# Kernel optimization log

Measured on AMD Instinct MI355X. Metric: run time of the kernel, lower is better.

The kernel has to match this reference:

```python
import jax, jax.numpy as jnp
import numpy as np

AUX_LOSS_WEIGHT = 0.01
TOP_K = 2


def setup_inputs() -> dict:
    key = jax.random.key(0)
    k0, k1, k2, k3, k4 = jax.random.split(key, 5)
    B, S, H, I, E = 4, 2048, 1024, 2816, 8
    scale = 0.02
    x = jax.random.normal(k0, (B, S, H), dtype=jnp.float32)
    Wr = jax.random.normal(k1, (H, E), dtype=jnp.float32) * scale   # router
    Wg = jax.random.normal(k2, (E, H, I), dtype=jnp.float32) * scale  # gate proj per expert
    Wu = jax.random.normal(k3, (E, H, I), dtype=jnp.float32) * scale  # up proj per expert
    Wd = jax.random.normal(k4, (E, I, H), dtype=jnp.float32) * scale  # down proj per expert
    return {"x": x, "Wr": Wr, "Wg": Wg, "Wu": Wu, "Wd": Wd}


def reference(x, Wr, Wg, Wu, Wd):
    B, S, H = x.shape
    E = Wr.shape[1]
    xf = x.reshape(-1, H)                      # [T, H]

    # Router: softmax -> top-k -> renormalize top-k weights
    logits = xf @ Wr                           # [T, E]
    probs = jax.nn.softmax(logits, axis=-1)
    vals, idx = jax.lax.top_k(probs, TOP_K)    # [T, K]
    vals = vals / (vals.sum(axis=-1, keepdims=True) + 1e-9)

    # Aux load-balancing loss (matches torch: mean prob * mean one-hot load)
    oh = jax.nn.one_hot(idx, E, dtype=xf.dtype)        # [T, K, E]
    expert_load = oh.sum(axis=1).mean(axis=0)          # [E]
    expert_prob = probs.mean(axis=0)                   # [E]
    router_loss = E * jnp.sum(expert_prob * expert_load) * AUX_LOSS_WEIGHT

    # Per-token combine weight for each expert: c[t,e] = sum_k vals[t,k] * (idx[t,k]==e)
    comb = jnp.einsum('tk,tke->te', vals, oh)          # [T, E]

    # Loop over the small fixed set of experts (dense SwiGLU, masked-weighted combine;
    # identical math to gather -> expert -> weighted index_add scatter)
    def expert_step(acc, ew):
        wg, wu, wd, ce = ew                            # [H,I], [H,I], [I,H], [T]
        h = jax.nn.silu(xf @ wg) * (xf @ wu)           # [T, I]
        return acc + (h @ wd) * ce[:, None], None

    out, _ = jax.lax.scan(expert_step, jnp.zeros_like(xf), (Wg, Wu, Wd, comb.T))
    return out.reshape(B, S, H), router_loss
```

## Files before the change

kernel.cpp:

```cpp
#include <hip/hip_runtime.h>
#include <stdint.h>

#define T_TOK 8192
#define HD    1024
#define ID    2816
#define NE    8
#define RCAP  17408
#define NYT   (RCAP / 128)

typedef __bf16 bf16x8 __attribute__((ext_vector_type(8)));
typedef float  f32x4  __attribute__((ext_vector_type(4)));

__device__ __forceinline__ unsigned short f2bf(float f) {
  union { float f; unsigned u; } v; v.f = f;
  unsigned r = v.u + 0x7FFFu + ((v.u >> 16) & 1u);
  return (unsigned short)(r >> 16);
}

__device__ __forceinline__ void gl16(const void* g, void* l) {
  __builtin_amdgcn_global_load_lds((__attribute__((address_space(1))) void*)g,
                                   (__attribute__((address_space(3))) void*)l,
                                   16, 0, 0);
}

__global__ void k_prep(const float* __restrict__ x, const float* __restrict__ Wr,
                       const float* __restrict__ Wg, const float* __restrict__ Wu,
                       const float* __restrict__ Wd,
                       unsigned short* __restrict__ Wgt, unsigned short* __restrict__ Wut,
                       unsigned short* __restrict__ Wdt, unsigned short* __restrict__ xb,
                       int* __restrict__ cnt, float* __restrict__ psum,
                       int* __restrict__ tok_e, float* __restrict__ tok_w) {
  __shared__ __align__(16) unsigned short tl[64 * 64];
  __shared__ float bp[NE];
  __shared__ int bc[NE];
  const int bid = blockIdx.x;
  const int t = threadIdx.x;

  if (bid < 16896) {
    const int m = bid / 704, bx = bid - m * 704;
    const float* src; unsigned short* dst; int R, C;
    if (m < 8)       { src = Wg + (size_t)m * HD * ID;        dst = Wgt + (size_t)m * HD * ID;        R = HD; C = ID; }
    else if (m < 16) { src = Wu + (size_t)(m - 8) * HD * ID;  dst = Wut + (size_t)(m - 8) * HD * ID;  R = HD; C = ID; }
    else             { src = Wd + (size_t)(m - 16) * HD * ID; dst = Wdt + (size_t)(m - 16) * HD * ID; R = ID; C = HD; }
    const int tc = C / 64;
    const int tr = bx / tc, tcc = bx % tc;
    const int r0 = tr * 64, c0 = tcc * 64;
    const int rb = t >> 4;
    const int c4 = t & 15;
    const float* sp = src + (size_t)(r0 + rb * 4) * C + c0 + c4 * 4;
    float4 v[4];
#pragma unroll
    for (int i = 0; i < 4; ++i) v[i] = *(const float4*)(sp + (size_t)i * C);
    const float* vf = (const float*)v;
#pragma unroll
    for (int q = 0; q < 4; ++q) {
      const int c = c4 * 4 + q;
      ushort4 o;
      o.x = f2bf(vf[0 * 4 + q]); o.y = f2bf(vf[1 * 4 + q]);
      o.z = f2bf(vf[2 * 4 + q]); o.w = f2bf(vf[3 * 4 + q]);
      *(ushort4*)&tl[c * 64 + ((rb ^ (c & 15)) * 4)] = o;
    }
    __syncthreads();
    const int orow = t >> 2, seg = t & 3;
    __align__(16) unsigned short tmp[16];
#pragma unroll
    for (int mI = 0; mI < 4; ++mI) {
      const int s = seg * 4 + mI;
      *(ushort4*)&tmp[mI * 4] = *(const ushort4*)&tl[orow * 64 + ((s ^ (orow & 15)) * 4)];
    }
    unsigned short* dp = dst + (size_t)(c0 + orow) * R + r0 + seg * 16;
    ((uint4*)dp)[0] = ((const uint4*)tmp)[0];
    ((uint4*)dp)[1] = ((const uint4*)tmp)[1];
  } else {
    const int b = bid - 16896;
    if (t < NE) { bp[t] = 0.f; bc[t] = 0; }
    __syncthreads();
    const int lane = t & 63, w = t >> 6;
    const int tok = b * 4 + w;
    float acc[NE] = {0.f, 0.f, 0.f, 0.f, 0.f, 0.f, 0.f, 0.f};
    for (int h = lane; h < HD; h += 64) {
      const float xv = x[(size_t)tok * HD + h];
      xb[(size_t)tok * HD + h] = f2bf(xv);
      const float4 w0 = *(const float4*)(Wr + h * 8);
      const float4 w1 = *(const float4*)(Wr + h * 8 + 4);
      acc[0] += xv * w0.x; acc[1] += xv * w0.y; acc[2] += xv * w0.z; acc[3] += xv * w0.w;
      acc[4] += xv * w1.x; acc[5] += xv * w1.y; acc[6] += xv * w1.z; acc[7] += xv * w1.w;
    }
#pragma unroll
    for (int e = 0; e < NE; ++e)
      for (int off = 32; off > 0; off >>= 1)
        acc[e] += __shfl_xor(acc[e], off, 64);
    if (lane == 0) {
      float mx = acc[0];
      for (int e = 1; e < NE; ++e) mx = fmaxf(mx, acc[e]);
      float p[NE], s = 0.f;
      for (int e = 0; e < NE; ++e) { p[e] = __expf(acc[e] - mx); s += p[e]; }
      const float inv = 1.f / s;
      for (int e = 0; e < NE; ++e) p[e] *= inv;
      int e0 = 0;
      for (int e = 1; e < NE; ++e) if (p[e] > p[e0]) e0 = e;
      int e1 = (e0 == 0) ? 1 : 0;
      for (int e = 0; e < NE; ++e) if (e != e0 && p[e] > p[e1]) e1 = e;
      const float v0 = p[e0], v1 = p[e1];
      const float invs = 1.f / (v0 + v1 + 1e-9f);
      tok_e[2 * tok] = e0;          tok_e[2 * tok + 1] = e1;
      tok_w[2 * tok] = v0 * invs;   tok_w[2 * tok + 1] = v1 * invs;
      atomicAdd(&bc[e0], 1); atomicAdd(&bc[e1], 1);
      for (int e = 0; e < NE; ++e) atomicAdd(&bp[e], p[e]);
    }
    __syncthreads();
    if (t < NE) { atomicAdd(&cnt[t], bc[t]); atomicAdd(&psum[t], bp[t]); }
  }
}

__global__ void k_offsets(const int* __restrict__ cnt, const float* __restrict__ psum,
                          int* __restrict__ offp, int* __restrict__ pair_tok,
                          float* __restrict__ pair_w, float* __restrict__ loss_out) {
  __shared__ int soff[NE + 1], scnt[NE];
  if (threadIdx.x == 0) {
    int o = 0;
    for (int e = 0; e < NE; ++e) {
      soff[e] = o; scnt[e] = cnt[e];
      o += (scnt[e] + 127) & ~127;
    }
    soff[NE] = o;
    for (int e = 0; e <= NE; ++e) offp[e] = soff[e];
    float loss = 0.f;
    for (int e = 0; e < NE; ++e) loss += psum[e] * (float)scnt[e];
    loss *= (float)NE * 0.01f / ((float)T_TOK * (float)T_TOK);
    *loss_out = loss;
  }
  __syncthreads();
  for (int e = 0; e < NE; ++e) {
    const int base = soff[e] + scnt[e];
    const int n = soff[e + 1] - base;
    for (int j = threadIdx.x; j < n; j += blockDim.x) {
      pair_tok[base + j] = -1;
      pair_w[base + j] = 0.f;
    }
  }
}

__global__ void k_scatter(const int* __restrict__ tok_e, const float* __restrict__ tok_w,
                          const int* __restrict__ offp, int* __restrict__ cursor,
                          int* __restrict__ pair_tok, float* __restrict__ pair_w,
                          int* __restrict__ inv_p) {
  const int t = blockIdx.x * 256 + threadIdx.x;
#pragma unroll
  for (int k = 0; k < 2; ++k) {
    const int e = tok_e[2 * t + k];
    const int pos = atomicAdd(&cursor[e], 1);
    const int idx = offp[e] + pos;
    pair_tok[idx] = t;
    pair_w[idx] = tok_w[2 * t + k];
    inv_p[2 * t + k] = idx;
  }
}

__launch_bounds__(256, 2)
__global__ void k_stage1(const unsigned short* __restrict__ xb,
                         const unsigned short* __restrict__ Wgt,
                         const unsigned short* __restrict__ Wut,
                         const int* __restrict__ offp,
                         const int* __restrict__ pair_tok,
                         unsigned short* __restrict__ act) {
  __shared__ __align__(16) unsigned short lA[8192];
  __shared__ __align__(16) unsigned short lBg[8192];
  __shared__ __align__(16) unsigned short lBu[8192];
  __shared__ int toks[128];

  const int wg = blockIdx.x;
  const int ytile = wg % NYT;
  const int i0 = (wg / NYT) * 128;
  const int row0 = ytile * 128;
  if (row0 >= offp[8]) return;
  int e = 0;
  while (offp[e + 1] <= row0) ++e;
  const int tid = threadIdx.x;
  if (tid < 128) {
    const int tk = pair_tok[row0 + tid];
    toks[tid] = tk < 0 ? 0 : tk;
  }
  __syncthreads();

  const int lane = tid & 63, w = tid >> 6;
  const unsigned short* gA[4];
  const unsigned short* gBg[4];
  const unsigned short* gBu[4];
  unsigned ldso[4];
  const unsigned short* wgtE = Wgt + (size_t)e * ID * HD;
  const unsigned short* wutE = Wut + (size_t)e * ID * HD;
#pragma unroll
  for (int j = 0; j < 4; ++j) {
    const int row = (w * 4 + j) * 8 + (lane >> 3);
    const int kb = (lane & 7) ^ (row & 7);
    gA[j]  = xb + (size_t)toks[row] * HD + kb * 8;
    gBg[j] = wgtE + (size_t)(i0 + row) * HD + kb * 8;
    gBu[j] = wutE + (size_t)(i0 + row) * HD + kb * 8;
    ldso[j] = (unsigned)(w * 4 + j) * 512u;
  }

  const f32x4 zero = {0.f, 0.f, 0.f, 0.f};
  f32x4 accg[4][4], accu[4][4];
#pragma unroll
  for (int a = 0; a < 4; ++a)
#pragma unroll
    for (int b = 0; b < 4; ++b) { accg[a][b] = zero; accu[a][b] = zero; }

  const int wm = (w & 1) * 64, wn = (w >> 1) * 64;
  const int colm = lane & 15, quad = lane >> 4;

  for (int kt = 0; kt < HD / 64; ++kt) {
    __syncthreads();
    const int ko = kt * 64;
#pragma unroll
    for (int j = 0; j < 4; ++j) {
      gl16(gA[j] + ko,  &lA[ldso[j]]);
      gl16(gBg[j] + ko, &lBg[ldso[j]]);
      gl16(gBu[j] + ko, &lBu[ldso[j]]);
    }
    __syncthreads();
#pragma unroll
    for (int kk = 0; kk < 2; ++kk) {
      const int kbl = kk * 4 + quad;
      bf16x8 af[4], bg[4], bu[4];
#pragma unroll
      for (int mf = 0; mf < 4; ++mf) {
        const int r = wm + mf * 16 + colm;
        af[mf] = *(const bf16x8*)&lA[r * 64 + ((kbl ^ (r & 7)) * 8)];
      }
#pragma unroll
      for (int nf = 0; nf < 4; ++nf) {
        const int r = wn + nf * 16 + colm;
        const int o = r * 64 + ((kbl ^ (r & 7)) * 8);
        bg[nf] = *(const bf16x8*)&lBg[o];
        bu[nf] = *(const bf16x8*)&lBu[o];
      }
#pragma unroll
      for (int mf = 0; mf < 4; ++mf)
#pragma unroll
        for (int nf = 0; nf < 4; ++nf) {
          accg[mf][nf] = __builtin_amdgcn_mfma_f32_16x16x32_bf16(af[mf], bg[nf], accg[mf][nf], 0, 0, 0);
          accu[mf][nf] = __builtin_amdgcn_mfma_f32_16x16x32_bf16(af[mf], bu[nf], accu[mf][nf], 0, 0, 0);
        }
    }
  }

#pragma unroll
  for (int mf = 0; mf < 4; ++mf) {
#pragma unroll
    for (int r = 0; r < 4; ++r) {
      const int orow = row0 + wm + mf * 16 + quad * 4 + r;
      unsigned short* arow = act + (size_t)orow * ID + i0 + wn + colm;
#pragma unroll
      for (int nf = 0; nf < 4; ++nf) {
        const float g = accg[mf][nf][r];
        const float u = accu[mf][nf][r];
        const float h = (g / (1.f + __expf(-g))) * u;
        arow[nf * 16] = f2bf(h);
      }
    }
  }
}

__launch_bounds__(256, 2)
__global__ void k_stage2(const unsigned short* __restrict__ act,
                         const unsigned short* __restrict__ Wdt,
                         const int* __restrict__ offp,
                         float* __restrict__ contrib) {
  __shared__ __align__(16) unsigned short lA[8192];
  __shared__ __align__(16) unsigned short lB[8192];

  const int wg = blockIdx.x;
  const int ytile = wg % NYT;
  const int h0 = (wg / NYT) * 128;
  const int row0 = ytile * 128;
  if (row0 >= offp[8]) return;
  int e = 0;
  while (offp[e + 1] <= row0) ++e;
  const int tid = threadIdx.x;
  const int lane = tid & 63, w = tid >> 6;
  const unsigned short* gA[4];
  const unsigned short* gB[4];
  unsigned ldso[4];
  const unsigned short* wdE = Wdt + (size_t)e * HD * ID;
#pragma unroll
  for (int j = 0; j < 4; ++j) {
    const int row = (w * 4 + j) * 8 + (lane >> 3);
    const int kb = (lane & 7) ^ (row & 7);
    gA[j] = act + (size_t)(row0 + row) * ID + kb * 8;
    gB[j] = wdE + (size_t)(h0 + row) * ID + kb * 8;
    ldso[j] = (unsigned)(w * 4 + j) * 512u;
  }

  const f32x4 zero = {0.f, 0.f, 0.f, 0.f};
  f32x4 acc[4][4];
#pragma unroll
  for (int a = 0; a < 4; ++a)
#pragma unroll
    for (int b = 0; b < 4; ++b) acc[a][b] = zero;

  const int wm = (w & 1) * 64, wn = (w >> 1) * 64;
  const int colm = lane & 15, quad = lane >> 4;

  for (int kt = 0; kt < ID / 64; ++kt) {
    __syncthreads();
    const int ko = kt * 64;
#pragma unroll
    for (int j = 0; j < 4; ++j) {
      gl16(gA[j] + ko, &lA[ldso[j]]);
      gl16(gB[j] + ko, &lB[ldso[j]]);
    }
    __syncthreads();
#pragma unroll
    for (int kk = 0; kk < 2; ++kk) {
      const int kbl = kk * 4 + quad;
      bf16x8 af[4], bf_[4];
#pragma unroll
      for (int mf = 0; mf < 4; ++mf) {
        const int r = wm + mf * 16 + colm;
        af[mf] = *(const bf16x8*)&lA[r * 64 + ((kbl ^ (r & 7)) * 8)];
      }
#pragma unroll
      for (int nf = 0; nf < 4; ++nf) {
        const int r = wn + nf * 16 + colm;
        bf_[nf] = *(const bf16x8*)&lB[r * 64 + ((kbl ^ (r & 7)) * 8)];
      }
#pragma unroll
      for (int mf = 0; mf < 4; ++mf)
#pragma unroll
        for (int nf = 0; nf < 4; ++nf)
          acc[mf][nf] = __builtin_amdgcn_mfma_f32_16x16x32_bf16(af[mf], bf_[nf], acc[mf][nf], 0, 0, 0);
    }
  }

#pragma unroll
  for (int mf = 0; mf < 4; ++mf) {
#pragma unroll
    for (int r = 0; r < 4; ++r) {
      const int lrow = wm + mf * 16 + quad * 4 + r;
      float* crow = contrib + (size_t)(row0 + lrow) * HD + h0 + wn + colm;
#pragma unroll
      for (int nf = 0; nf < 4; ++nf)
        crow[nf * 16] = acc[mf][nf][r];
    }
  }
}

__global__ void k_combine(const float* __restrict__ contrib, const int* __restrict__ inv_p,
                          const float* __restrict__ tok_w, float* __restrict__ out) {
  const int t = blockIdx.x;
  const int h4 = threadIdx.x;
  const int p0 = inv_p[2 * t], p1 = inv_p[2 * t + 1];
  const float w0 = tok_w[2 * t], w1 = tok_w[2 * t + 1];
  const float4 a = ((const float4*)(contrib + (size_t)p0 * HD))[h4];
  const float4 b = ((const float4*)(contrib + (size_t)p1 * HD))[h4];
  float4 o;
  o.x = w0 * a.x + w1 * b.x;
  o.y = w0 * a.y + w1 * b.y;
  o.z = w0 * a.z + w1 * b.z;
  o.w = w0 * a.w + w1 * b.w;
  ((float4*)(out + (size_t)t * HD))[h4] = o;
}

extern "C" void kernel_launch(void* const* d_in, const int* in_sizes, int n_in,
                              void* d_out, int out_size, void* d_ws, size_t ws_size,
                              hipStream_t stream) {
  const float* x  = (const float*)d_in[0];
  const float* Wr = (const float*)d_in[1];
  const float* Wg = (const float*)d_in[2];
  const float* Wu = (const float*)d_in[3];
  const float* Wd = (const float*)d_in[4];
  float* out = (float*)d_out;

  char* ws = (char*)d_ws;
  const size_t off_xb  = 256;
  const size_t sz_xb   = (size_t)T_TOK * HD * 2;
  const size_t sz_w    = (size_t)NE * HD * ID * 2;
  const size_t off_wgt = off_xb + sz_xb;
  const size_t off_wut = off_wgt + sz_w;
  const size_t off_wdt = off_wut + sz_w;
  const size_t off_act = off_wdt + sz_w;
  const size_t sz_act  = (size_t)RCAP * ID * 2;
  const size_t off_ptk = off_act + sz_act;
  const size_t off_pw  = off_ptk + (size_t)RCAP * 4;
  const size_t off_te  = off_pw + (size_t)RCAP * 4;
  const size_t off_tw  = off_te + (size_t)T_TOK * 2 * 4;
  const size_t off_ip  = off_tw + (size_t)T_TOK * 2 * 4;
  const size_t need    = off_ip + (size_t)T_TOK * 2 * 4;
  if (ws_size < need) return;

  int*   cnt    = (int*)(ws + 0);
  float* psum   = (float*)(ws + 32);
  int*   cursor = (int*)(ws + 64);
  int*   offp   = (int*)(ws + 96);
  unsigned short* xb  = (unsigned short*)(ws + off_xb);
  unsigned short* Wgt = (unsigned short*)(ws + off_wgt);
  unsigned short* Wut = (unsigned short*)(ws + off_wut);
  unsigned short* Wdt = (unsigned short*)(ws + off_wdt);
  unsigned short* act = (unsigned short*)(ws + off_act);
  int*   pair_tok = (int*)(ws + off_ptk);
  float* pair_w   = (float*)(ws + off_pw);
  int*   tok_e    = (int*)(ws + off_te);
  float* tok_w    = (float*)(ws + off_tw);
  int*   inv_p    = (int*)(ws + off_ip);
  float* contrib  = (float*)(ws + off_wgt);

  hipMemsetAsync(ws, 0, 256, stream);

  k_prep<<<16896 + T_TOK / 4, 256, 0, stream>>>(x, Wr, Wg, Wu, Wd, Wgt, Wut, Wdt, xb,
                                                cnt, psum, tok_e, tok_w);
  k_offsets<<<1, 256, 0, stream>>>(cnt, psum, offp, pair_tok, pair_w, out + (size_t)T_TOK * HD);
  k_scatter<<<T_TOK / 256, 256, 0, stream>>>(tok_e, tok_w, offp, cursor, pair_tok, pair_w, inv_p);
  k_stage1<<<(ID / 128) * NYT, 256, 0, stream>>>(xb, Wgt, Wut, offp, pair_tok, act);
  k_stage2<<<(HD / 128) * NYT, 256, 0, stream>>>(act, Wdt, offp, contrib);
  k_combine<<<T_TOK, 256, 0, stream>>>(contrib, inv_p, tok_w, out);
}
```

Baseline: 820.8 us.

## Software-pipeline stage2 GEMM with multi-buffered LDS and hand-placed waitcnts

Rewrites the down-projection GEMM loop so global-to-LDS loads for later half-k-tiles are issued while MFMAs run on earlier ones. It uses a four-slot LDS ring with explicit vmcnt/lgkmcnt waits, sched barriers and setprio around the MFMA block. The block index is also remapped (XCD-style swizzle) so neighbouring blocks share the same expert weights, and stage1 switches to a 2D grid with the row tile on the y axis. In exchange the code takes on more LDS (64KB per block), a hand-tuned wait schedule that is fragile, and a new swizzle pattern whose correctness depends on matching the read side.

```diff
diff --git a/kernel.cpp b/kernel.cpp
--- a/kernel.cpp
+++ b/kernel.cpp
@@ -22,6 +22,17 @@
                                    (__attribute__((address_space(3))) void*)l,
                                    16, 0, 0);
 }
+
+__device__ __forceinline__ bf16x8 dsr128(unsigned a) {
+  bf16x8 r;
+  asm volatile("ds_read_b128 %0, %1" : "=v"(r) : "v"(a));
+  return r;
+}
+
+#define S2VM(n) asm volatile("s_waitcnt vmcnt(" #n ")")
+#define S2LG0   asm volatile("s_waitcnt lgkmcnt(0)")
+#define SBAR0   __builtin_amdgcn_sched_barrier(0)
+#define HBAR    __builtin_amdgcn_s_barrier()
 
 __global__ void k_prep(const float* __restrict__ x, const float* __restrict__ Wr,
                        const float* __restrict__ Wg, const float* __restrict__ Wu,
@@ -169,13 +180,11 @@
   __shared__ __align__(16) unsigned short lBu[8192];
   __shared__ int toks[128];
 
-  const int wg = blockIdx.x;
-  const int ytile = wg % NYT;
-  const int i0 = (wg / NYT) * 128;
-  const int row0 = ytile * 128;
+  const int row0 = blockIdx.y * 128;
   if (row0 >= offp[8]) return;
   int e = 0;
   while (offp[e + 1] <= row0) ++e;
+  const int i0 = blockIdx.x * 128;
   const int tid = threadIdx.x;
   if (tid < 128) {
     const int tk = pair_tok[row0 + tid];
@@ -263,35 +272,68 @@
   }
 }
 
+#define STG2(b, h, t) do { \
+  const int go_ = (t) * 64 + (h) * 32; \
+  char* lb_ = (char*)smem + ((b) * 16384 + (h) * 8192) + wdst; \
+  gl16(srcA0 + go_, lb_); \
+  gl16(srcA1 + go_, lb_ + 4096); \
+  gl16(srcB0 + go_, lb_ + 32768); \
+  gl16(srcB1 + go_, lb_ + 32768 + 4096); \
+} while (0)
+
+#define S2_PHASE(b, h, STAGE, VMW) do { \
+  bf16x8 af[4], bf_[4]; \
+  _Pragma("unroll") for (int i_ = 0; i_ < 4; ++i_) \
+    af[i_] = dsr128(aRd + (b) * 16384 + (h) * 8192 + i_ * 1024); \
+  _Pragma("unroll") for (int i_ = 0; i_ < 4; ++i_) \
+    bf_[i_] = dsr128(bRd + (b) * 16384 + (h) * 8192 + i_ * 1024); \
+  STAGE; \
+  SBAR0; HBAR; S2LG0; SBAR0; \
+  __builtin_amdgcn_s_setprio(1); \
+  _Pragma("unroll") for (int mf_ = 0; mf_ < 4; ++mf_) \
+    _Pragma("unroll") for (int nf_ = 0; nf_ < 4; ++nf_) \
+      acc[mf_][nf_] = __builtin_amdgcn_mfma_f32_16x16x32_bf16(af[mf_], bf_[nf_], acc[mf_][nf_], 0, 0, 0); \
+  __builtin_amdgcn_s_setprio(0); \
+  SBAR0; \
+  VMW; \
+  HBAR; \
+} while (0)
+
 __launch_bounds__(256, 2)
 __global__ void k_stage2(const unsigned short* __restrict__ act,
                          const unsigned short* __restrict__ Wdt,
                          const int* __restrict__ offp,
                          float* __restrict__ contrib) {
-  __shared__ __align__(16) unsigned short lA[8192];
-  __shared__ __align__(16) unsigned short lB[8192];
-
-  const int wg = blockIdx.x;
-  const int ytile = wg % NYT;
-  const int h0 = (wg / NYT) * 128;
+  __shared__ __align__(16) unsigned short smem[32768];
+
+  int wg = blockIdx.x;
+  wg = (wg & 7) * 136 + (wg >> 3);
+  const int htile = wg & 7, ytile = wg >> 3;
   const int row0 = ytile * 128;
   if (row0 >= offp[8]) return;
   int e = 0;
   while (offp[e + 1] <= row0) ++e;
+  const int h0 = htile * 128;
+
   const int tid = threadIdx.x;
-  const int lane = tid & 63, w = tid >> 6;
-  const unsigned short* gA[4];
-  const unsigned short* gB[4];
-  unsigned ldso[4];
+  const int l = tid & 63, w = tid >> 6;
+  const int colm = l & 15, quad = l >> 4;
+  const int wm = (w & 1) * 64, wn = (w >> 1) * 64;
+
+  const int rr = w * 16 + (l >> 2);
+  const int ks = (l & 3) ^ ((l >> 3) & 3);
   const unsigned short* wdE = Wdt + (size_t)e * HD * ID;
-#pragma unroll
-  for (int j = 0; j < 4; ++j) {
-    const int row = (w * 4 + j) * 8 + (lane >> 3);
-    const int kb = (lane & 7) ^ (row & 7);
-    gA[j] = act + (size_t)(row0 + row) * ID + kb * 8;
-    gB[j] = wdE + (size_t)(h0 + row) * ID + kb * 8;
-    ldso[j] = (unsigned)(w * 4 + j) * 512u;
-  }
+  const unsigned short* srcA0 = act + (size_t)(row0 + rr) * ID + ks * 8;
+  const unsigned short* srcA1 = act + (size_t)(row0 + 64 + rr) * ID + ks * 8;
+  const unsigned short* srcB0 = wdE + (size_t)(h0 + rr) * ID + ks * 8;
+  const unsigned short* srcB1 = wdE + (size_t)(h0 + 64 + rr) * ID + ks * 8;
+  const int wdst = w * 1024;
+
+  const unsigned ldsBase =
+      (unsigned)(uintptr_t)(__attribute__((address_space(3))) unsigned short*)smem;
+  const int slotB = (quad ^ ((colm >> 1) & 3)) * 16;
+  const unsigned aRd = ldsBase + (unsigned)((wm + colm) * 64 + slotB);
+  const unsigned bRd = ldsBase + 32768u + (unsigned)((wn + colm) * 64 + slotB);
 
   const f32x4 zero = {0.f, 0.f, 0.f, 0.f};
   f32x4 acc[4][4];
@@ -300,38 +342,24 @@
 #pragma unroll
     for (int b = 0; b < 4; ++b) acc[a][b] = zero;
 
-  const int wm = (w & 1) * 64, wn = (w >> 1) * 64;
-  const int colm = lane & 15, quad = lane >> 4;
-
-  for (int kt = 0; kt < ID / 64; ++kt) {
-    __syncthreads();
-    const int ko = kt * 64;
-#pragma unroll
-    for (int j = 0; j < 4; ++j) {
-      gl16(gA[j] + ko, &lA[ldso[j]]);
-      gl16(gB[j] + ko, &lB[ldso[j]]);
-    }
-    __syncthreads();
-#pragma unroll
-    for (int kk = 0; kk < 2; ++kk) {
-      const int kbl = kk * 4 + quad;
-      bf16x8 af[4], bf_[4];
-#pragma unroll
-      for (int mf = 0; mf < 4; ++mf) {
-        const int r = wm + mf * 16 + colm;
-        af[mf] = *(const bf16x8*)&lA[r * 64 + ((kbl ^ (r & 7)) * 8)];
-      }
-#pragma unroll
-      for (int nf = 0; nf < 4; ++nf) {
-        const int r = wn + nf * 16 + colm;
-        bf_[nf] = *(const bf16x8*)&lB[r * 64 + ((kbl ^ (r & 7)) * 8)];
-      }
-#pragma unroll
-      for (int mf = 0; mf < 4; ++mf)
-#pragma unroll
-        for (int nf = 0; nf < 4; ++nf)
-          acc[mf][nf] = __builtin_amdgcn_mfma_f32_16x16x32_bf16(af[mf], bf_[nf], acc[mf][nf], 0, 0, 0);
-    }
+  STG2(0, 0, 0);
+  STG2(0, 1, 0);
+  STG2(1, 0, 1);
+  S2VM(4); HBAR;
+
+  for (int T = 0; T < 44; T += 2) {
+    S2_PHASE(0, 0,
+      { if (T + 1 < 44) STG2(1, 1, T + 1); },
+      { if (T + 1 < 44) { S2VM(8); } else { S2VM(0); } });
+    S2_PHASE(0, 1,
+      { if (T + 2 < 44) STG2(0, 0, T + 2); },
+      { if (T + 2 < 44) { S2VM(8); } else if (T + 1 < 44) { S2VM(4); } else { S2VM(0); } });
+    S2_PHASE(1, 0,
+      { if (T + 2 < 44) STG2(0, 1, T + 2); },
+      { if (T + 2 < 44) { S2VM(8); } else { S2VM(0); } });
+    S2_PHASE(1, 1,
+      { if (T + 3 < 44) STG2(1, 0, T + 3); },
+      { if (T + 3 < 44) { S2VM(8); } else if (T + 2 < 44) { S2VM(4); } else { S2VM(0); } });
   }
 
 #pragma unroll
@@ -412,7 +440,7 @@
                                                 cnt, psum, tok_e, tok_w);
   k_offsets<<<1, 256, 0, stream>>>(cnt, psum, offp, pair_tok, pair_w, out + (size_t)T_TOK * HD);
   k_scatter<<<T_TOK / 256, 256, 0, stream>>>(tok_e, tok_w, offp, cursor, pair_tok, pair_w, inv_p);
-  k_stage1<<<(ID / 128) * NYT, 256, 0, stream>>>(xb, Wgt, Wut, offp, pair_tok, act);
-  k_stage2<<<(HD / 128) * NYT, 256, 0, stream>>>(act, Wdt, offp, contrib);
+  k_stage1<<<dim3(ID / 128, NYT), 256, 0, stream>>>(xb, Wgt, Wut, offp, pair_tok, act);
+  k_stage2<<<NYT * (HD / 128), 256, 0, stream>>>(act, Wdt, offp, contrib);
   k_combine<<<T_TOK, 256, 0, stream>>>(contrib, inv_p, tok_w, out);
 }
```

New measurement: 791.1 us. 1.04x faster.
